# Kernel optimization log

Hardware: AMD Instinct MI355X
Metric: run time of the kernel (lower is better)

## Reference

```python
import jax, jax.numpy as jnp
import numpy as np

N_NODES = 100_000
N_EDGES = 1_600_000
HEADS = 3
DIMS = [6, 8, 16, 32]  # in -> conv1 -> conv2 -> conv3 out_feats


def _edge_gat(x, ef, src, dst, W, We, al, ar, ae, b, n_nodes):
    """DGL EdgeGATConv: edge feats modulate attention logits; messages are alpha * W h_src."""
    H, D = al.shape
    ft = (x @ W.T).reshape(n_nodes, H, D)          # [N,H,D] projected node feats
    fe = (ef @ We.T).reshape(-1, H, D)             # [E,H,D] projected edge feats
    el = jnp.sum(ft * al, axis=-1)                 # [N,H]
    er = jnp.sum(ft * ar, axis=-1)                 # [N,H]
    ee = jnp.sum(fe * ae, axis=-1)                 # [E,H]
    e = jax.nn.leaky_relu(el[src] + er[dst] + ee, 0.2)  # [E,H] (DGL default slope 0.2)
    # segment softmax over incoming edges of each dst node
    m = jax.ops.segment_max(e, dst, num_segments=n_nodes)
    m = jnp.where(jnp.isfinite(m), m, 0.0)         # zero-in-degree nodes
    ex = jnp.exp(e - m[dst])
    denom = jax.ops.segment_sum(ex, dst, num_segments=n_nodes)
    a = ex / jnp.maximum(denom[dst], 1e-9)         # [E,H]
    msg = a[:, :, None] * ft[src]                  # [E,H,D]
    out = jax.ops.segment_sum(msg, dst, num_segments=n_nodes)  # [N,H,D]
    return out + b.reshape(1, H, D)


def setup_inputs() -> dict:
    key = jax.random.key(0)
    ks = jax.random.split(key, 32)
    d = {
        "node_feats": jax.random.normal(ks[0], (N_NODES, DIMS[0]), jnp.float32),
        "edge_feats": jax.random.uniform(ks[1], (N_EDGES, 1), jnp.float32),
        "src": jax.random.randint(ks[2], (N_EDGES,), 0, N_NODES, jnp.int32),
        "dst": jax.random.randint(ks[3], (N_EDGES,), 0, N_NODES, jnp.int32),
    }
    ki = 4
    for i in range(3):
        fin, fout = DIMS[i], DIMS[i + 1]
        s = 1.0 / np.sqrt(fin)
        d[f"W{i+1}"] = jax.random.normal(ks[ki], (HEADS * fout, fin), jnp.float32) * s; ki += 1
        d[f"We{i+1}"] = jax.random.normal(ks[ki], (HEADS * fout, 1), jnp.float32); ki += 1
        d[f"al{i+1}"] = jax.random.normal(ks[ki], (HEADS, fout), jnp.float32) * 0.1; ki += 1
        d[f"ar{i+1}"] = jax.random.normal(ks[ki], (HEADS, fout), jnp.float32) * 0.1; ki += 1
        d[f"ae{i+1}"] = jax.random.normal(ks[ki], (HEADS, fout), jnp.float32) * 0.1; ki += 1
        d[f"b{i+1}"] = jnp.zeros((HEADS * fout,), jnp.float32)
    for name, (fo, fi) in [("l1", (16, 32)), ("l2", (4, 16)), ("l3", (1, 4)), ("l4", (1, HEADS))]:
        s = 1.0 / np.sqrt(fi)
        d[name + "w"] = jax.random.uniform(ks[ki], (fo, fi), jnp.float32, -s, s); ki += 1
        d[name + "b"] = jax.random.uniform(ks[ki], (fo,), jnp.float32, -s, s); ki += 1
    return d


def reference(node_feats, edge_feats, src, dst,
              W1, We1, al1, ar1, ae1, b1,
              W2, We2, al2, ar2, ae2, b2,
              W3, We3, al3, ar3, ae3, b3,
              l1w, l1b, l2w, l2b, l3w, l3b, l4w, l4b):
    n = node_feats.shape[0]
    h1 = _edge_gat(node_feats, edge_feats, src, dst, W1, We1, al1, ar1, ae1, b1, n)  # [N,3,8]
    h2 = _edge_gat(h1.mean(axis=1), edge_feats, src, dst, W2, We2, al2, ar2, ae2, b2, n)  # [N,3,16]
    h3 = _edge_gat(h2.mean(axis=1), edge_feats, src, dst, W3, We3, al3, ar3, ae3, b3, n)  # [N,3,32]
    # per-(node,head) MLP head: 32 -> 16 -> 4 -> 1
    x = jax.nn.leaky_relu(h3 @ l1w.T + l1b, 0.01)
    x = jax.nn.leaky_relu(x @ l2w.T + l2b, 0.01)
    x = x @ l3w.T + l3b                            # [N,3,1]
    feats = x.reshape(n, -1) @ l4w.T + l4b         # [N,1] combine heads
    return jnp.max(feats, axis=0)                  # [1]
```

## Files before the change

### kernel.cpp

```cpp
#include <hip/hip_runtime.h>
#include <hip/hip_bf16.h>
#include <hip/hip_fp16.h>

#define HEADS 3

union HU { uint4 u; __half2 h[4]; };

__global__ void prep_ce_kernel(const float* __restrict__ We1, const float* __restrict__ ae1,
                               const float* __restrict__ We2, const float* __restrict__ ae2,
                               const float* __restrict__ We3, const float* __restrict__ ae3,
                               float* __restrict__ ce) {
    int t = threadIdx.x;
    if (t >= 9) return;
    int l = t / 3, h = t % 3;
    const float* We = (l == 0) ? We1 : (l == 1) ? We2 : We3;
    const float* ae = (l == 0) ? ae1 : (l == 1) ? ae2 : ae3;
    int D = (l == 0) ? 8 : (l == 1) ? 16 : 32;
    float s = 0.f;
    for (int d = 0; d < D; d++) s += We[h * D + d] * ae[h * D + d];
    ce[t] = s;
}

__global__ void hist_kernel(const int* __restrict__ dst, int* __restrict__ deg, int E) {
    int tid = blockIdx.x * blockDim.x + threadIdx.x;
    if (tid < E) atomicAdd(&deg[dst[tid]], 1);
}

#define SCAN_BLK 1024
__global__ void scan1_kernel(const int* __restrict__ deg, int* __restrict__ row_ptr,
                             int* __restrict__ partials, int N) {
    __shared__ int sm[SCAN_BLK];
    int t = threadIdx.x;
    int g = blockIdx.x * SCAN_BLK + t;
    int v = (g < N) ? deg[g] : 0;
    sm[t] = v;
    __syncthreads();
    for (int off = 1; off < SCAN_BLK; off <<= 1) {
        int x = (t >= off) ? sm[t - off] : 0;
        __syncthreads();
        sm[t] += x;
        __syncthreads();
    }
    if (g < N) row_ptr[g] = sm[t] - v;
    if (t == SCAN_BLK - 1) partials[blockIdx.x] = sm[t];
}

__global__ void scan2_kernel(int* __restrict__ partials, int NB) {
    __shared__ int sm[128];
    int t = threadIdx.x;
    int v = (t < NB) ? partials[t] : 0;
    sm[t] = v;
    __syncthreads();
    for (int off = 1; off < 128; off <<= 1) {
        int x = (t >= off) ? sm[t - off] : 0;
        __syncthreads();
        sm[t] += x;
        __syncthreads();
    }
    if (t < NB) partials[t] = sm[t] - v;
    if (t == 127) partials[NB] = sm[127];
}

__global__ void scan3_kernel(int* __restrict__ row_ptr, const int* __restrict__ partials,
                             int N, int NB) {
    int g = blockIdx.x * SCAN_BLK + threadIdx.x;
    if (g < N) row_ptr[g] += partials[blockIdx.x];
    if (blockIdx.x == 0 && threadIdx.x == 0) row_ptr[N] = partials[NB];
}

__global__ void scatter_kernel(const int* __restrict__ src, const int* __restrict__ dst,
                               const float* __restrict__ ef, const int* __restrict__ row_ptr,
                               int* __restrict__ cnt, int2* __restrict__ erec, int E) {
    int tid = blockIdx.x * blockDim.x + threadIdx.x;
    if (tid >= E) return;
    int d = dst[tid];
    int pos = row_ptr[d] + atomicAdd(&cnt[d], 1);
    int2 r;
    r.x = src[tid];
    r.y = __float_as_int(ef[tid]);
    erec[pos] = r;
}

template <int FIN, int D, bool MEAN_PREV>
__launch_bounds__(256)
__global__ void node_kernel(const float* __restrict__ xin,
                            const float* __restrict__ W,
                            const float* __restrict__ al,
                            const float* __restrict__ ar,
                            __half* __restrict__ ft,
                            float* __restrict__ el, float* __restrict__ er,
                            int N) {
    int tid = blockIdx.x * blockDim.x + threadIdx.x;
    if (tid >= N * HEADS) return;
    int n = tid / HEADS, h = tid % HEADS;
    float x[FIN];
    if (MEAN_PREV) {
        #pragma unroll
        for (int k = 0; k < FIN; k++)
            x[k] = (xin[(n * HEADS + 0) * FIN + k] +
                    xin[(n * HEADS + 1) * FIN + k] +
                    xin[(n * HEADS + 2) * FIN + k]) * (1.0f / 3.0f);
    } else {
        #pragma unroll
        for (int k = 0; k < FIN; k++) x[k] = xin[n * FIN + k];
    }
    float fv[D];
    float e_l = 0.f, e_r = 0.f;
    #pragma unroll
    for (int d = 0; d < D; d++) {
        const float* wr = &W[(h * D + d) * FIN];
        float f = 0.f;
        #pragma unroll
        for (int k = 0; k < FIN; k++) f += x[k] * wr[k];
        fv[d] = f;
        e_l += f * al[h * D + d];
        e_r += f * ar[h * D + d];
    }
    uint4* dst16 = (uint4*)(ft + (size_t)tid * D);
    #pragma unroll
    for (int q = 0; q < D / 8; q++) {
        HU u;
        #pragma unroll
        for (int j = 0; j < 4; j++)
            u.h[j] = __floats2half2_rn(fv[q * 8 + 2 * j], fv[q * 8 + 2 * j + 1]);
        dst16[q] = u.u;
    }
    el[tid] = e_l;
    er[tid] = e_r;
}

template <int D>
__launch_bounds__(256)
__global__ void agg_kernel(const int* __restrict__ row_ptr, const int2* __restrict__ erec,
                           const __half* __restrict__ ft,
                           const float* __restrict__ el, const float* __restrict__ er,
                           const float* __restrict__ ce,
                           const float* __restrict__ b,
                           float* __restrict__ out,
                           int N) {
    int w = threadIdx.x >> 6;
    int l = threadIdx.x & 63;
    int wl = l / 6;
    int rem = l - wl * 6;
    int s = rem >= 3 ? 1 : 0;
    int h = rem - s * 3;
    int n = (blockIdx.x * 4 + w) * 10 + wl;
    bool active = (wl < 10) && (n < N);

    float m = -3.0e38f, ssum = 0.f;
    float msg[D];
    #pragma unroll
    for (int d = 0; d < D; d++) msg[d] = 0.f;
    int unit = n * HEADS + h;
    float ceh = ce[h];

    if (active) {
        int beg = row_ptr[n], end = row_ptr[n + 1];
        int cnt = end - beg;
        int half = (cnt + 1) >> 1;
        int es = beg + s * half;
        int ee = s ? end : (beg + half);
        float ern = er[unit];

        int e = es;
        for (; e + 3 < ee; e += 4) {
            int2 r0 = erec[e + 0], r1 = erec[e + 1], r2 = erec[e + 2], r3 = erec[e + 3];
            float v0 = el[r0.x * HEADS + h] + ern + __int_as_float(r0.y) * ceh;
            float v1 = el[r1.x * HEADS + h] + ern + __int_as_float(r1.y) * ceh;
            float v2 = el[r2.x * HEADS + h] + ern + __int_as_float(r2.y) * ceh;
            float v3 = el[r3.x * HEADS + h] + ern + __int_as_float(r3.y) * ceh;
            v0 = v0 > 0.f ? v0 : 0.2f * v0;
            v1 = v1 > 0.f ? v1 : 0.2f * v1;
            v2 = v2 > 0.f ? v2 : 0.2f * v2;
            v3 = v3 > 0.f ? v3 : 0.2f * v3;
            float cm = fmaxf(fmaxf(v0, v1), fmaxf(v2, v3));
            if (cm > m) {
                float sc = __expf(m - cm);
                ssum *= sc;
                #pragma unroll
                for (int d = 0; d < D; d++) msg[d] *= sc;
                m = cm;
            }
            float x0 = __expf(v0 - m), x1 = __expf(v1 - m);
            float x2 = __expf(v2 - m), x3 = __expf(v3 - m);
            ssum += (x0 + x1) + (x2 + x3);
            const uint4* f0 = (const uint4*)(ft + ((size_t)r0.x * HEADS + h) * D);
            const uint4* f1 = (const uint4*)(ft + ((size_t)r1.x * HEADS + h) * D);
            const uint4* f2 = (const uint4*)(ft + ((size_t)r2.x * HEADS + h) * D);
            const uint4* f3 = (const uint4*)(ft + ((size_t)r3.x * HEADS + h) * D);
            #pragma unroll
            for (int q = 0; q < D / 8; q++) {
                HU a0, a1, a2, a3;
                a0.u = f0[q]; a1.u = f1[q]; a2.u = f2[q]; a3.u = f3[q];
                #pragma unroll
                for (int j = 0; j < 4; j++) {
                    float2 p0 = __half22float2(a0.h[j]);
                    float2 p1 = __half22float2(a1.h[j]);
                    float2 p2 = __half22float2(a2.h[j]);
                    float2 p3 = __half22float2(a3.h[j]);
                    msg[q * 8 + 2 * j + 0] += x0 * p0.x + x1 * p1.x + x2 * p2.x + x3 * p3.x;
                    msg[q * 8 + 2 * j + 1] += x0 * p0.y + x1 * p1.y + x2 * p2.y + x3 * p3.y;
                }
            }
        }
        for (; e < ee; e++) {
            int2 r = erec[e];
            float v = el[r.x * HEADS + h] + ern + __int_as_float(r.y) * ceh;
            v = v > 0.f ? v : 0.2f * v;
            if (v > m) {
                float sc = __expf(m - v);
                ssum *= sc;
                #pragma unroll
                for (int d = 0; d < D; d++) msg[d] *= sc;
                m = v;
            }
            float x = __expf(v - m);
            ssum += x;
            const uint4* fr = (const uint4*)(ft + ((size_t)r.x * HEADS + h) * D);
            #pragma unroll
            for (int q = 0; q < D / 8; q++) {
                HU a; a.u = fr[q];
                #pragma unroll
                for (int j = 0; j < 4; j++) {
                    float2 p = __half22float2(a.h[j]);
                    msg[q * 8 + 2 * j + 0] += x * p.x;
                    msg[q * 8 + 2 * j + 1] += x * p.y;
                }
            }
        }
    }

    int pl = (s ? (l - 3) : (l + 3)) & 63;
    float om = __shfl(m, pl);
    float osum = __shfl(ssum, pl);
    float M = fmaxf(m, om);
    float sA = __expf(m - M);
    float sB = __expf(om - M);
    float tot = ssum * sA + osum * sB;
    float inv = 1.0f / fmaxf(tot, 1e-9f);
    #pragma unroll
    for (int d = 0; d < D; d++)
        msg[d] = msg[d] * sA + __shfl(msg[d], pl) * sB;

    if (active) {
        int lo = s * (D / 2);
        float* ob = out + (size_t)unit * D + lo;
        #pragma unroll
        for (int d = 0; d < D / 2; d += 4) {
            float4 v;
            v.x = msg[lo + d + 0] * inv + b[h * D + lo + d + 0];
            v.y = msg[lo + d + 1] * inv + b[h * D + lo + d + 1];
            v.z = msg[lo + d + 2] * inv + b[h * D + lo + d + 2];
            v.w = msg[lo + d + 3] * inv + b[h * D + lo + d + 3];
            *(float4*)(ob + d) = v;
        }
    }
}

__global__ void mlp_max_kernel(const float* __restrict__ h3,
                               const float* __restrict__ l1w, const float* __restrict__ l1b,
                               const float* __restrict__ l2w, const float* __restrict__ l2b,
                               const float* __restrict__ l3w, const float* __restrict__ l3b,
                               const float* __restrict__ l4w, const float* __restrict__ l4b,
                               unsigned int* __restrict__ maxkey, int N) {
    int tid = blockIdx.x * blockDim.x + threadIdx.x;
    float feat = -3.0e38f;
    if (tid < N) {
        float acc = l4b[0];
        #pragma unroll
        for (int h = 0; h < HEADS; h++) {
            const float4* vp = (const float4*)&h3[((size_t)tid * HEADS + h) * 32];
            float v[32];
            #pragma unroll
            for (int q = 0; q < 8; q++) {
                float4 t = vp[q];
                v[q * 4 + 0] = t.x; v[q * 4 + 1] = t.y; v[q * 4 + 2] = t.z; v[q * 4 + 3] = t.w;
            }
            float y1[16];
            #pragma unroll
            for (int i = 0; i < 16; i++) {
                float s = l1b[i];
                const float* w = &l1w[i * 32];
                #pragma unroll
                for (int k = 0; k < 32; k++) s += v[k] * w[k];
                y1[i] = s > 0.f ? s : 0.01f * s;
            }
            float y2[4];
            #pragma unroll
            for (int i = 0; i < 4; i++) {
                float s = l2b[i];
                const float* w = &l2w[i * 16];
                #pragma unroll
                for (int k = 0; k < 16; k++) s += y1[k] * w[k];
                y2[i] = s > 0.f ? s : 0.01f * s;
            }
            float y3 = l3b[0];
            #pragma unroll
            for (int k = 0; k < 4; k++) y3 += y2[k] * l3w[k];
            acc += y3 * l4w[h];
        }
        feat = acc;
    }
    #pragma unroll
    for (int off = 32; off > 0; off >>= 1)
        feat = fmaxf(feat, __shfl_down(feat, off));
    if ((threadIdx.x & 63) == 0) {
        unsigned int u = __float_as_uint(feat);
        unsigned int key = (u & 0x80000000u) ? ~u : (u | 0x80000000u);
        atomicMax(maxkey, key);
    }
}

__global__ void finalize_kernel(const unsigned int* __restrict__ maxkey, float* __restrict__ out) {
    unsigned int key = *maxkey;
    unsigned int u = (key & 0x80000000u) ? (key & 0x7FFFFFFFu) : ~key;
    out[0] = __uint_as_float(u);
}

extern "C" void kernel_launch(void* const* d_in, const int* in_sizes, int n_in,
                              void* d_out, int out_size, void* d_ws, size_t ws_size,
                              hipStream_t stream) {
    const float* node_feats = (const float*)d_in[0];
    const float* edge_feats = (const float*)d_in[1];
    const int* src = (const int*)d_in[2];
    const int* dst = (const int*)d_in[3];
    const float* W1  = (const float*)d_in[4];
    const float* We1 = (const float*)d_in[5];
    const float* al1 = (const float*)d_in[6];
    const float* ar1 = (const float*)d_in[7];
    const float* ae1 = (const float*)d_in[8];
    const float* b1  = (const float*)d_in[9];
    const float* W2  = (const float*)d_in[10];
    const float* We2 = (const float*)d_in[11];
    const float* al2 = (const float*)d_in[12];
    const float* ar2 = (const float*)d_in[13];
    const float* ae2 = (const float*)d_in[14];
    const float* b2  = (const float*)d_in[15];
    const float* W3  = (const float*)d_in[16];
    const float* We3 = (const float*)d_in[17];
    const float* al3 = (const float*)d_in[18];
    const float* ar3 = (const float*)d_in[19];
    const float* ae3 = (const float*)d_in[20];
    const float* b3  = (const float*)d_in[21];
    const float* l1w = (const float*)d_in[22];
    const float* l1b = (const float*)d_in[23];
    const float* l2w = (const float*)d_in[24];
    const float* l2b = (const float*)d_in[25];
    const float* l3w = (const float*)d_in[26];
    const float* l3b = (const float*)d_in[27];
    const float* l4w = (const float*)d_in[28];
    const float* l4b = (const float*)d_in[29];

    const int N = in_sizes[0] / 6;
    const int E = in_sizes[2];
    const int NB = (N + SCAN_BLK - 1) / SCAN_BLK;

    char* ws = (char*)d_ws;
    size_t off = 0;
    auto alloc = [&](size_t bytes) -> void* {
        void* p = ws + off;
        off = (off + bytes + 255) & ~(size_t)255;
        return p;
    };
    int* deg            = (int*)alloc((size_t)N * 4);
    int* cnt            = (int*)alloc((size_t)N * 4);
    unsigned int* mkey  = (unsigned int*)alloc(4);
    size_t zero_bytes   = off;
    int* row_ptr        = (int*)alloc((size_t)(N + 1) * 4);
    int* partials       = (int*)alloc((size_t)(NB + 1) * 4);
    int2* erec          = (int2*)alloc((size_t)E * 8);
    __half* ft          = (__half*)alloc((size_t)N * 96 * 2);
    float* outb         = (float*)alloc((size_t)N * 96 * 4);
    float* el           = (float*)alloc((size_t)N * 3 * 4);
    float* er           = (float*)alloc((size_t)N * 3 * 4);
    float* ce           = (float*)alloc(9 * 4);

    hipMemsetAsync(d_ws, 0, zero_bytes, stream);

    prep_ce_kernel<<<1, 16, 0, stream>>>(We1, ae1, We2, ae2, We3, ae3, ce);
    hist_kernel<<<(E + 255) / 256, 256, 0, stream>>>(dst, deg, E);
    scan1_kernel<<<NB, SCAN_BLK, 0, stream>>>(deg, row_ptr, partials, N);
    scan2_kernel<<<1, 128, 0, stream>>>(partials, NB);
    scan3_kernel<<<NB, SCAN_BLK, 0, stream>>>(row_ptr, partials, N, NB);
    scatter_kernel<<<(E + 255) / 256, 256, 0, stream>>>(src, dst, edge_feats, row_ptr, cnt,
                                                        erec, E);

    const int NH = N * HEADS;
    const int gb = (NH + 255) / 256;
    const int gb_agg = (N + 39) / 40;

    node_kernel<6, 8, false><<<gb, 256, 0, stream>>>(node_feats, W1, al1, ar1, ft, el, er, N);
    agg_kernel<8><<<gb_agg, 256, 0, stream>>>(row_ptr, erec, ft, el, er, ce + 0, b1, outb, N);
    node_kernel<8, 16, true><<<gb, 256, 0, stream>>>(outb, W2, al2, ar2, ft, el, er, N);
    agg_kernel<16><<<gb_agg, 256, 0, stream>>>(row_ptr, erec, ft, el, er, ce + 3, b2, outb, N);
    node_kernel<16, 32, true><<<gb, 256, 0, stream>>>(outb, W3, al3, ar3, ft, el, er, N);
    agg_kernel<32><<<gb_agg, 256, 0, stream>>>(row_ptr, erec, ft, el, er, ce + 6, b3, outb, N);

    mlp_max_kernel<<<(N + 255) / 256, 256, 0, stream>>>(outb, l1w, l1b, l2w, l2b, l3w, l3b,
                                                        l4w, l4b, mkey, N);
    finalize_kernel<<<1, 1, 0, stream>>>(mkey, (float*)d_out);
}
```

Baseline: 520.9 us.

## Fuse head-mean and MLP-max epilogues into aggregation, reuse hist ranks for scatter

The aggregation kernel now averages the three heads with cross-lane shuffles and writes only a mean vector of N*D floats, replacing the full N*3*D output that the next node kernel had to read back. The last layer's aggregation computes the MLP head and max reduction in place, so the separate mlp_max kernel and its read of the full h3 buffer are gone. The histogram kernel records each edge's atomic rank so the scatter needs no second atomic pass, and the scatter writes edge records with nontemporal stores. In exchange there are extra shuffles and register use in the aggregation epilogue, plus an E-sized rank buffer.

```diff
diff --git a/kernel.cpp b/kernel.cpp
--- a/kernel.cpp
+++ b/kernel.cpp
@@ -21,9 +21,10 @@
     ce[t] = s;
 }
 
-__global__ void hist_kernel(const int* __restrict__ dst, int* __restrict__ deg, int E) {
+__global__ void hist_rank_kernel(const int* __restrict__ dst, int* __restrict__ deg,
+                                 int* __restrict__ rank, int E) {
     int tid = blockIdx.x * blockDim.x + threadIdx.x;
-    if (tid < E) atomicAdd(&deg[dst[tid]], 1);
+    if (tid < E) rank[tid] = atomicAdd(&deg[dst[tid]], 1);
 }
 
 #define SCAN_BLK 1024
@@ -70,18 +71,18 @@
 
 __global__ void scatter_kernel(const int* __restrict__ src, const int* __restrict__ dst,
                                const float* __restrict__ ef, const int* __restrict__ row_ptr,
-                               int* __restrict__ cnt, int2* __restrict__ erec, int E) {
+                               const int* __restrict__ rank, int2* __restrict__ erec, int E) {
     int tid = blockIdx.x * blockDim.x + threadIdx.x;
     if (tid >= E) return;
     int d = dst[tid];
-    int pos = row_ptr[d] + atomicAdd(&cnt[d], 1);
-    int2 r;
-    r.x = src[tid];
-    r.y = __float_as_int(ef[tid]);
-    erec[pos] = r;
-}
-
-template <int FIN, int D, bool MEAN_PREV>
+    int pos = row_ptr[d] + rank[tid];
+    union { int2 r; long long ll; } u;
+    u.r.x = src[tid];
+    u.r.y = __float_as_int(ef[tid]);
+    __builtin_nontemporal_store(u.ll, (long long*)&erec[pos]);
+}
+
+template <int FIN, int D>
 __launch_bounds__(256)
 __global__ void node_kernel(const float* __restrict__ xin,
                             const float* __restrict__ W,
@@ -94,16 +95,8 @@
     if (tid >= N * HEADS) return;
     int n = tid / HEADS, h = tid % HEADS;
     float x[FIN];
-    if (MEAN_PREV) {
-        #pragma unroll
-        for (int k = 0; k < FIN; k++)
-            x[k] = (xin[(n * HEADS + 0) * FIN + k] +
-                    xin[(n * HEADS + 1) * FIN + k] +
-                    xin[(n * HEADS + 2) * FIN + k]) * (1.0f / 3.0f);
-    } else {
-        #pragma unroll
-        for (int k = 0; k < FIN; k++) x[k] = xin[n * FIN + k];
-    }
+    #pragma unroll
+    for (int k = 0; k < FIN; k++) x[k] = xin[n * FIN + k];
     float fv[D];
     float e_l = 0.f, e_r = 0.f;
     #pragma unroll
@@ -129,14 +122,19 @@
     er[tid] = e_r;
 }
 
-template <int D>
+template <int D, int EPI>
 __launch_bounds__(256)
 __global__ void agg_kernel(const int* __restrict__ row_ptr, const int2* __restrict__ erec,
                            const __half* __restrict__ ft,
                            const float* __restrict__ el, const float* __restrict__ er,
                            const float* __restrict__ ce,
                            const float* __restrict__ b,
-                           float* __restrict__ out,
+                           float* __restrict__ xmean,
+                           const float* __restrict__ l1w, const float* __restrict__ l1b,
+                           const float* __restrict__ l2w, const float* __restrict__ l2b,
+                           const float* __restrict__ l3w, const float* __restrict__ l3b,
+                           const float* __restrict__ l4w, const float* __restrict__ l4b,
+                           unsigned int* __restrict__ maxkey,
                            int N) {
     int w = threadIdx.x >> 6;
     int l = threadIdx.x & 63;
@@ -238,76 +236,65 @@
     float sB = __expf(om - M);
     float tot = ssum * sA + osum * sB;
     float inv = 1.0f / fmaxf(tot, 1e-9f);
+    float o[D];
     #pragma unroll
     for (int d = 0; d < D; d++)
-        msg[d] = msg[d] * sA + __shfl(msg[d], pl) * sB;
-
-    if (active) {
-        int lo = s * (D / 2);
-        float* ob = out + (size_t)unit * D + lo;
-        #pragma unroll
-        for (int d = 0; d < D / 2; d += 4) {
-            float4 v;
-            v.x = msg[lo + d + 0] * inv + b[h * D + lo + d + 0];
-            v.y = msg[lo + d + 1] * inv + b[h * D + lo + d + 1];
-            v.z = msg[lo + d + 2] * inv + b[h * D + lo + d + 2];
-            v.w = msg[lo + d + 3] * inv + b[h * D + lo + d + 3];
-            *(float4*)(ob + d) = v;
-        }
-    }
-}
-
-__global__ void mlp_max_kernel(const float* __restrict__ h3,
-                               const float* __restrict__ l1w, const float* __restrict__ l1b,
-                               const float* __restrict__ l2w, const float* __restrict__ l2b,
-                               const float* __restrict__ l3w, const float* __restrict__ l3b,
-                               const float* __restrict__ l4w, const float* __restrict__ l4b,
-                               unsigned int* __restrict__ maxkey, int N) {
-    int tid = blockIdx.x * blockDim.x + threadIdx.x;
-    float feat = -3.0e38f;
-    if (tid < N) {
-        float acc = l4b[0];
-        #pragma unroll
-        for (int h = 0; h < HEADS; h++) {
-            const float4* vp = (const float4*)&h3[((size_t)tid * HEADS + h) * 32];
-            float v[32];
-            #pragma unroll
-            for (int q = 0; q < 8; q++) {
-                float4 t = vp[q];
-                v[q * 4 + 0] = t.x; v[q * 4 + 1] = t.y; v[q * 4 + 2] = t.z; v[q * 4 + 3] = t.w;
-            }
-            float y1[16];
-            #pragma unroll
-            for (int i = 0; i < 16; i++) {
-                float s = l1b[i];
-                const float* w = &l1w[i * 32];
-                #pragma unroll
-                for (int k = 0; k < 32; k++) s += v[k] * w[k];
-                y1[i] = s > 0.f ? s : 0.01f * s;
-            }
-            float y2[4];
-            #pragma unroll
-            for (int i = 0; i < 4; i++) {
-                float s = l2b[i];
-                const float* w = &l2w[i * 16];
-                #pragma unroll
-                for (int k = 0; k < 16; k++) s += y1[k] * w[k];
-                y2[i] = s > 0.f ? s : 0.01f * s;
-            }
-            float y3 = l3b[0];
-            #pragma unroll
-            for (int k = 0; k < 4; k++) y3 += y2[k] * l3w[k];
-            acc += y3 * l4w[h];
-        }
-        feat = acc;
-    }
-    #pragma unroll
-    for (int off = 32; off > 0; off >>= 1)
-        feat = fmaxf(feat, __shfl_down(feat, off));
-    if ((threadIdx.x & 63) == 0) {
-        unsigned int u = __float_as_uint(feat);
-        unsigned int key = (u & 0x80000000u) ? ~u : (u | 0x80000000u);
-        atomicMax(maxkey, key);
+        o[d] = (msg[d] * sA + __shfl(msg[d], pl) * sB) * inv + b[h * D + d];
+
+    if (EPI == 0) {
+        int g0 = wl * 6 + s * 3;
+        #pragma unroll
+        for (int d = 0; d < D; d++)
+            o[d] = (__shfl(o[d], g0) + __shfl(o[d], g0 + 1) + __shfl(o[d], g0 + 2)) * (1.0f / 3.0f);
+        if (active && h == 0) {
+            int lo = s * (D / 2);
+            float* ob = xmean + (size_t)n * D + lo;
+            #pragma unroll
+            for (int d = 0; d < D / 2; d += 4) {
+                float4 v;
+                v.x = o[lo + d + 0]; v.y = o[lo + d + 1];
+                v.z = o[lo + d + 2]; v.w = o[lo + d + 3];
+                *(float4*)(ob + d) = v;
+            }
+        }
+    } else {
+        float y1[8];
+        #pragma unroll
+        for (int i = 0; i < 8; i++) {
+            int row = s * 8 + i;
+            float acc1 = l1b[row];
+            const float* wr = &l1w[row * 32];
+            #pragma unroll
+            for (int k = 0; k < 32; k++) acc1 += o[k] * wr[k];
+            y1[i] = acc1 > 0.f ? acc1 : 0.01f * acc1;
+        }
+        float y2[4];
+        #pragma unroll
+        for (int i = 0; i < 4; i++) {
+            float p = 0.f;
+            const float* wr = &l2w[i * 16 + s * 8];
+            #pragma unroll
+            for (int k = 0; k < 8; k++) p += y1[k] * wr[k];
+            p += __shfl(p, pl);
+            p += l2b[i];
+            y2[i] = p > 0.f ? p : 0.01f * p;
+        }
+        float y3 = l3b[0];
+        #pragma unroll
+        for (int k = 0; k < 4; k++) y3 += y2[k] * l3w[k];
+        int g0 = wl * 6 + s * 3;
+        float feat = l4b[0];
+        #pragma unroll
+        for (int hh = 0; hh < 3; hh++) feat += __shfl(y3, g0 + hh) * l4w[hh];
+        if (!active) feat = -3.0e38f;
+        #pragma unroll
+        for (int off = 32; off > 0; off >>= 1)
+            feat = fmaxf(feat, __shfl_down(feat, off));
+        if (l == 0) {
+            unsigned int u = __float_as_uint(feat);
+            unsigned int key = (u & 0x80000000u) ? ~u : (u | 0x80000000u);
+            atomicMax(maxkey, key);
+        }
     }
 }
 
@@ -363,14 +350,14 @@
         return p;
     };
     int* deg            = (int*)alloc((size_t)N * 4);
-    int* cnt            = (int*)alloc((size_t)N * 4);
     unsigned int* mkey  = (unsigned int*)alloc(4);
     size_t zero_bytes   = off;
+    int* rank           = (int*)alloc((size_t)E * 4);
     int* row_ptr        = (int*)alloc((size_t)(N + 1) * 4);
     int* partials       = (int*)alloc((size_t)(NB + 1) * 4);
     int2* erec          = (int2*)alloc((size_t)E * 8);
     __half* ft          = (__half*)alloc((size_t)N * 96 * 2);
-    float* outb         = (float*)alloc((size_t)N * 96 * 4);
+    float* xmean        = (float*)alloc((size_t)N * 16 * 4);
     float* el           = (float*)alloc((size_t)N * 3 * 4);
     float* er           = (float*)alloc((size_t)N * 3 * 4);
     float* ce           = (float*)alloc(9 * 4);
@@ -378,25 +365,31 @@
     hipMemsetAsync(d_ws, 0, zero_bytes, stream);
 
     prep_ce_kernel<<<1, 16, 0, stream>>>(We1, ae1, We2, ae2, We3, ae3, ce);
-    hist_kernel<<<(E + 255) / 256, 256, 0, stream>>>(dst, deg, E);
+    hist_rank_kernel<<<(E + 255) / 256, 256, 0, stream>>>(dst, deg, rank, E);
     scan1_kernel<<<NB, SCAN_BLK, 0, stream>>>(deg, row_ptr, partials, N);
     scan2_kernel<<<1, 128, 0, stream>>>(partials, NB);
     scan3_kernel<<<NB, SCAN_BLK, 0, stream>>>(row_ptr, partials, N, NB);
-    scatter_kernel<<<(E + 255) / 256, 256, 0, stream>>>(src, dst, edge_feats, row_ptr, cnt,
+    scatter_kernel<<<(E + 255) / 256, 256, 0, stream>>>(src, dst, edge_feats, row_ptr, rank,
                                                         erec, E);
 
     const int NH = N * HEADS;
     const int gb = (NH + 255) / 256;
     const int gb_agg = (N + 39) / 40;
 
-    node_kernel<6, 8, false><<<gb, 256, 0, stream>>>(node_feats, W1, al1, ar1, ft, el, er, N);
-    agg_kernel<8><<<gb_agg, 256, 0, stream>>>(row_ptr, erec, ft, el, er, ce + 0, b1, outb, N);
-    node_kernel<8, 16, true><<<gb, 256, 0, stream>>>(outb, W2, al2, ar2, ft, el, er, N);
-    agg_kernel<16><<<gb_agg, 256, 0, stream>>>(row_ptr, erec, ft, el, er, ce + 3, b2, outb, N);
-    node_kernel<16, 32, true><<<gb, 256, 0, stream>>>(outb, W3, al3, ar3, ft, el, er, N);
-    agg_kernel<32><<<gb_agg, 256, 0, stream>>>(row_ptr, erec, ft, el, er, ce + 6, b3, outb, N);
-
-    mlp_max_kernel<<<(N + 255) / 256, 256, 0, stream>>>(outb, l1w, l1b, l2w, l2b, l3w, l3b,
-                                                        l4w, l4b, mkey, N);
+    node_kernel<6, 8><<<gb, 256, 0, stream>>>(node_feats, W1, al1, ar1, ft, el, er, N);
+    agg_kernel<8, 0><<<gb_agg, 256, 0, stream>>>(row_ptr, erec, ft, el, er, ce + 0, b1, xmean,
+                                                 nullptr, nullptr, nullptr, nullptr,
+                                                 nullptr, nullptr, nullptr, nullptr,
+                                                 nullptr, N);
+    node_kernel<8, 16><<<gb, 256, 0, stream>>>(xmean, W2, al2, ar2, ft, el, er, N);
+    agg_kernel<16, 0><<<gb_agg, 256, 0, stream>>>(row_ptr, erec, ft, el, er, ce + 3, b2, xmean,
+                                                  nullptr, nullptr, nullptr, nullptr,
+                                                  nullptr, nullptr, nullptr, nullptr,
+                                                  nullptr, N);
+    node_kernel<16, 32><<<gb, 256, 0, stream>>>(xmean, W3, al3, ar3, ft, el, er, N);
+    agg_kernel<32, 1><<<gb_agg, 256, 0, stream>>>(row_ptr, erec, ft, el, er, ce + 6, b3, nullptr,
+                                                  l1w, l1b, l2w, l2b, l3w, l3b, l4w, l4b,
+                                                  mkey, N);
+
     finalize_kernel<<<1, 1, 0, stream>>>(mkey, (float*)d_out);
 }
```

Result: faster. 498.2 us (-4.4%).
